# Optimization experiments

Hardware: AMD Instinct MI355X
Metric: run time of the kernel (lower is better)

The kernel has to match this reference:

```python
import jax, jax.numpy as jnp
import numpy as np

B, S, D, H = 2, 2048, 1024, 16
HD = D // H
NEG = -9e15


def setup_inputs() -> dict:
    key = jax.random.key(0)
    ks = jax.random.split(key, 4)
    x = jax.random.normal(ks[0], (B, S, D), dtype=jnp.float32)
    # causal mask, broadcastable over batch and heads
    mask = jnp.tril(jnp.ones((S, S), dtype=jnp.int32))[None, None]
    W_qkv = jax.random.normal(ks[1], (D, 3 * D), dtype=jnp.float32) * (1.0 / np.sqrt(D))
    b_qkv = jnp.zeros((3 * D,), dtype=jnp.float32)
    W_out = jax.random.normal(ks[2], (D, D), dtype=jnp.float32) * (1.0 / np.sqrt(D))
    b_out = jnp.zeros((D,), dtype=jnp.float32)
    return {"x": x, "mask": mask, "W_qkv": W_qkv, "b_qkv": b_qkv,
            "W_out": W_out, "b_out": b_out}


def reference(x, mask, W_qkv, b_qkv, W_out, b_out):
    b, s, _ = x.shape
    qkv = x @ W_qkv + b_qkv                       # [B,S,3D]
    qkv = qkv.reshape(b, s, H, 3 * HD)            # per-head interleaved qkv
    qkv = jnp.transpose(qkv, (0, 2, 1, 3))        # [B,H,S,3*HD]
    q, k, v = jnp.split(qkv, 3, axis=-1)          # each [B,H,S,HD]
    scores = jnp.einsum('bhqd,bhkd->bhqk', q, k) / np.sqrt(HD)
    scores = jnp.where(mask == 0, jnp.float32(NEG), scores)
    attn = jax.nn.softmax(scores, axis=-1)
    out = jnp.einsum('bhqk,bhkd->bhqd', attn, v)  # [B,H,S,HD]
    out = jnp.transpose(out, (0, 2, 1, 3)).reshape(b, s, H * HD)
    return out @ W_out + b_out
```

## Files before the change

kernel.cpp:

```cpp
#include <hip/hip_runtime.h>
#include <math.h>

constexpr int Bb = 2, Ss = 2048, Dd = 1024, Hh = 16, HDd = 64;

typedef __attribute__((ext_vector_type(8))) short bf16x8;
typedef __attribute__((ext_vector_type(4))) float f32x4;
typedef __attribute__((ext_vector_type(8))) unsigned short u16x8;
typedef __attribute__((ext_vector_type(4))) unsigned short u16x4;

__device__ __forceinline__ unsigned short bf16_rn(float f) {
  unsigned int u = __float_as_uint(f);
  u += 0x7fffu + ((u >> 16) & 1u);
  return (unsigned short)(u >> 16);
}
__device__ __forceinline__ float bf16_f(unsigned short h) {
  return __uint_as_float(((unsigned int)h) << 16);
}

__global__ __launch_bounds__(256) void split_f32(
    const float* __restrict__ in, unsigned short* __restrict__ hi,
    unsigned short* __restrict__ lo, int n8) {
  int i = blockIdx.x * 256 + threadIdx.x;
  if (i >= n8) return;
  const float4* p = (const float4*)in + (size_t)i * 2;
  float4 a = p[0], b = p[1];
  float v[8] = {a.x, a.y, a.z, a.w, b.x, b.y, b.z, b.w};
  u16x8 h, l;
  #pragma unroll
  for (int j = 0; j < 8; j++) {
    unsigned short hb = bf16_rn(v[j]);
    h[j] = hb;
    l[j] = bf16_rn(v[j] - bf16_f(hb));
  }
  *(u16x8*)(hi + (size_t)i * 8) = h;
  *(u16x8*)(lo + (size_t)i * 8) = l;
}

__global__ __launch_bounds__(256) void transpose_split_f32(
    const float* __restrict__ W, unsigned short* __restrict__ Thi,
    unsigned short* __restrict__ Tlo, int K, int N) {
  __shared__ float tile[32][33];
  int n0 = blockIdx.x * 32, k0 = blockIdx.y * 32;
  int t = threadIdx.x;
  #pragma unroll
  for (int p = 0; p < 4; p++) {
    int idx = t + p * 256;
    int kk = idx >> 5, nn = idx & 31;
    tile[kk][nn] = W[(size_t)(k0 + kk) * N + n0 + nn];
  }
  __syncthreads();
  #pragma unroll
  for (int p = 0; p < 4; p++) {
    int idx = t + p * 256;
    int nn = idx >> 5, kk = idx & 31;
    float v = tile[kk][nn];
    unsigned short hb = bf16_rn(v);
    size_t o = (size_t)(n0 + nn) * K + k0 + kk;
    Thi[o] = hb;
    Tlo[o] = bf16_rn(v - bf16_f(hb));
  }
}

typedef __attribute__((address_space(3))) unsigned int lds_u32;
typedef const __attribute__((address_space(1))) unsigned int glb_u32;
__device__ __forceinline__ void gload16(const void* g, void* l) {
  __builtin_amdgcn_global_load_lds((glb_u32*)g, (lds_u32*)l, 16, 0, 0);
}

#define GEMM_CORE(KD)                                                          \
  __shared__ unsigned short lds[4 * 4096];                                     \
  const int tid = threadIdx.x;                                                 \
  const int lane = tid & 63, wid = tid >> 6;                                   \
  const int m0 = blockIdx.y * 128, n0 = blockIdx.x * 128;                      \
  const int wrow = wid >> 1, wcol = wid & 1;                                   \
  const int lrow = lane & 15, g = lane >> 4;                                   \
  const int o0 = wid * 128 + lane, o1 = o0 + 64;                               \
  const int r0 = o0 >> 2, G0 = (o0 & 3) ^ ((r0 >> 1) & 3);                     \
  const int r1 = o1 >> 2, G1 = (o1 & 3) ^ ((r1 >> 1) & 3);                     \
  const unsigned short* sA0h = Ahi + (size_t)(m0 + r0) * KD + G0 * 8;          \
  const unsigned short* sA1h = Ahi + (size_t)(m0 + r1) * KD + G1 * 8;          \
  const unsigned short* sA0l = Alo + (size_t)(m0 + r0) * KD + G0 * 8;          \
  const unsigned short* sA1l = Alo + (size_t)(m0 + r1) * KD + G1 * 8;          \
  const unsigned short* sB0h = Bhi + (size_t)(n0 + r0) * KD + G0 * 8;          \
  const unsigned short* sB1h = Bhi + (size_t)(n0 + r1) * KD + G1 * 8;          \
  const unsigned short* sB0l = Blo + (size_t)(n0 + r0) * KD + G0 * 8;          \
  const unsigned short* sB1l = Blo + (size_t)(n0 + r1) * KD + G1 * 8;          \
  unsigned short* dA0h = lds + 0 + wid * 1024;                                 \
  unsigned short* dA1h = dA0h + 512;                                           \
  unsigned short* dA0l = lds + 4096 + wid * 1024;                              \
  unsigned short* dA1l = dA0l + 512;                                           \
  unsigned short* dB0h = lds + 8192 + wid * 1024;                              \
  unsigned short* dB1h = dB0h + 512;                                           \
  unsigned short* dB0l = lds + 12288 + wid * 1024;                             \
  unsigned short* dB1l = dB0l + 512;                                           \
  int offA[4], offB[4];                                                        \
  _Pragma("unroll")                                                            \
  for (int m = 0; m < 4; m++) {                                                \
    int row = wrow * 64 + m * 16 + lrow;                                       \
    offA[m] = row * 32 + ((g ^ ((row >> 1) & 3)) * 8);                         \
  }                                                                            \
  _Pragma("unroll")                                                            \
  for (int n = 0; n < 4; n++) {                                                \
    int row = wcol * 64 + n * 16 + lrow;                                       \
    offB[n] = row * 32 + ((g ^ ((row >> 1) & 3)) * 8);                         \
  }                                                                            \
  f32x4 acc[4][4];                                                             \
  _Pragma("unroll")                                                            \
  for (int m = 0; m < 4; m++)                                                  \
    _Pragma("unroll")                                                          \
    for (int n = 0; n < 4; n++) acc[m][n] = (f32x4){0.f, 0.f, 0.f, 0.f};       \
  for (int k0 = 0; k0 < KD; k0 += 32) {                                        \
    gload16(sA0h + k0, dA0h); gload16(sA1h + k0, dA1h);                        \
    gload16(sA0l + k0, dA0l); gload16(sA1l + k0, dA1l);                        \
    gload16(sB0h + k0, dB0h); gload16(sB1h + k0, dB1h);                        \
    gload16(sB0l + k0, dB0l); gload16(sB1l + k0, dB1l);                        \
    __syncthreads();                                                           \
    bf16x8 ah[4], al[4], bh[4], bl[4];                                         \
    _Pragma("unroll")                                                          \
    for (int m = 0; m < 4; m++) {                                              \
      ah[m] = *(const bf16x8*)(lds + 0 + offA[m]);                             \
      al[m] = *(const bf16x8*)(lds + 4096 + offA[m]);                          \
    }                                                                          \
    _Pragma("unroll")                                                          \
    for (int n = 0; n < 4; n++) {                                              \
      bh[n] = *(const bf16x8*)(lds + 8192 + offB[n]);                          \
      bl[n] = *(const bf16x8*)(lds + 12288 + offB[n]);                         \
    }                                                                          \
    _Pragma("unroll")                                                          \
    for (int m = 0; m < 4; m++)                                                \
      _Pragma("unroll")                                                        \
      for (int n = 0; n < 4; n++) {                                            \
        acc[m][n] = __builtin_amdgcn_mfma_f32_16x16x32_bf16(ah[m], bh[n], acc[m][n], 0, 0, 0); \
        acc[m][n] = __builtin_amdgcn_mfma_f32_16x16x32_bf16(ah[m], bl[n], acc[m][n], 0, 0, 0); \
        acc[m][n] = __builtin_amdgcn_mfma_f32_16x16x32_bf16(al[m], bh[n], acc[m][n], 0, 0, 0); \
      }                                                                        \
    __syncthreads();                                                           \
  }

template<int KD>
__global__ __launch_bounds__(256) void gemm_split_bf16(
    const unsigned short* __restrict__ Ahi, const unsigned short* __restrict__ Alo,
    const unsigned short* __restrict__ Bhi, const unsigned short* __restrict__ Blo,
    const float* __restrict__ bias, float* __restrict__ C, int N)
{
  GEMM_CORE(KD)
  #pragma unroll
  for (int n = 0; n < 4; n++) {
    int gcol = n0 + wcol * 64 + n * 16 + lrow;
    float bv = bias[gcol];
    #pragma unroll
    for (int m = 0; m < 4; m++) {
      f32x4 a = acc[m][n];
      #pragma unroll
      for (int r = 0; r < 4; r++) {
        int grow = m0 + wrow * 64 + m * 16 + g * 4 + r;
        C[(size_t)grow * N + gcol] = a[r] + bv;
      }
    }
  }
}

template<int KD>
__global__ __launch_bounds__(256) void gemm_qkv(
    const unsigned short* __restrict__ Ahi, const unsigned short* __restrict__ Alo,
    const unsigned short* __restrict__ Bhi, const unsigned short* __restrict__ Blo,
    const float* __restrict__ bias,
    unsigned short* __restrict__ Qh, unsigned short* __restrict__ Ql,
    unsigned short* __restrict__ Kh, unsigned short* __restrict__ Kl,
    unsigned short* __restrict__ Vth, unsigned short* __restrict__ Vtl)
{
  GEMM_CORE(KD)
  const int bidx = m0 >> 11;
  const int sbase = (m0 & 2047) + wrow * 64 + g * 4;
  #pragma unroll
  for (int n = 0; n < 4; n++) {
    int gcol = n0 + wcol * 64 + n * 16 + lrow;
    unsigned hh = (unsigned)gcol / 192u;
    int inner = gcol - (int)hh * 192;
    int part = inner >> 6;
    int d = inner & 63;
    float bv = bias[gcol];
    size_t base = (size_t)(bidx * 16 + (int)hh) * 131072;
    #pragma unroll
    for (int m = 0; m < 4; m++) {
      f32x4 a = acc[m][n];
      int s0 = sbase + m * 16;
      if (part == 0) {
        #pragma unroll
        for (int r = 0; r < 4; r++) {
          float v = (a[r] + bv) * 0.18033688011112042f;
          unsigned short hi = bf16_rn(v);
          size_t ix = base + (size_t)(s0 + r) * 64 + d;
          Qh[ix] = hi; Ql[ix] = bf16_rn(v - bf16_f(hi));
        }
      } else if (part == 1) {
        #pragma unroll
        for (int r = 0; r < 4; r++) {
          float v = a[r] + bv;
          unsigned short hi = bf16_rn(v);
          size_t ix = base + (size_t)(s0 + r) * 64 + d;
          Kh[ix] = hi; Kl[ix] = bf16_rn(v - bf16_f(hi));
        }
      } else {
        u16x4 hv, lv;
        #pragma unroll
        for (int r = 0; r < 4; r++) {
          float v = a[r] + bv;
          hv[r] = bf16_rn(v);
          lv[r] = bf16_rn(v - bf16_f(hv[r]));
        }
        size_t ix = base + (size_t)d * 2048 + s0;
        *(u16x4*)(Vth + ix) = hv;
        *(u16x4*)(Vtl + ix) = lv;
      }
    }
  }
}

__global__ __launch_bounds__(256) void flash_attn_mfma(
    const unsigned short* __restrict__ Qh, const unsigned short* __restrict__ Ql,
    const unsigned short* __restrict__ Kh, const unsigned short* __restrict__ Kl,
    const unsigned short* __restrict__ Vth, const unsigned short* __restrict__ Vtl,
    unsigned short* __restrict__ atthi, unsigned short* __restrict__ attlo)
{
  const int qt = (int)gridDim.x - 1 - (int)blockIdx.x;
  const int h = blockIdx.y, b = blockIdx.z;
  const int bh = b * Hh + h;
  const int q0 = qt * 128;
  const int tid = threadIdx.x, lane = tid & 63, wid = tid >> 6;
  const int q0w = q0 + wid * 32;
  const int lrow = lane & 15, lg = lane >> 4;

  __shared__ unsigned short KH[2][4096], KL[2][4096], VH[2][4096], VL[2][4096];
  __shared__ unsigned short Pbuf[4][2048];

  const size_t hb = (size_t)bh * 131072;
  const unsigned short* qhb = Qh + hb;
  const unsigned short* qlb = Ql + hb;
  const unsigned short* khb = Kh + hb;
  const unsigned short* klb = Kl + hb;
  const unsigned short* vhb = Vth + hb;
  const unsigned short* vlb = Vtl + hb;

  bf16x8 qfh[2][2], qfl[2][2];
  #pragma unroll
  for (int mi = 0; mi < 2; mi++)
    #pragma unroll
    for (int ks = 0; ks < 2; ks++) {
      int off = (q0w + mi * 16 + lrow) * 64 + ks * 32 + lg * 8;
      qfh[mi][ks] = *(const bf16x8*)(qhb + off);
      qfl[mi][ks] = *(const bf16x8*)(qlb + off);
    }

  int offK[4][2], offP[2][2];
  #pragma unroll
  for (int ci = 0; ci < 4; ci++)
    #pragma unroll
    for (int ks = 0; ks < 2; ks++) {
      int row = ci * 16 + lrow;
      offK[ci][ks] = row * 64 + (((ks * 4 + lg) ^ (row & 7)) * 8);
    }
  #pragma unroll
  for (int mi = 0; mi < 2; mi++)
    #pragma unroll
    for (int ks = 0; ks < 2; ks++) {
      int row = mi * 16 + lrow;
      offP[mi][ks] = row * 64 + (((ks * 4 + lg) ^ (row & 7)) * 8);
    }

  const int o0 = tid, o1 = tid + 256;
  const int sr0 = o0 >> 3, sg0 = ((o0 & 7) ^ (sr0 & 7)) * 8;
  const int sr1 = o1 >> 3, sg1 = ((o1 & 7) ^ (sr1 & 7)) * 8;

  float m_[2][4], l_[2][4];
  f32x4 oacc[2][4];
  #pragma unroll
  for (int mi = 0; mi < 2; mi++)
    #pragma unroll
    for (int r = 0; r < 4; r++) { m_[mi][r] = -INFINITY; l_[mi][r] = 0.f; }
  #pragma unroll
  for (int mi = 0; mi < 2; mi++)
    #pragma unroll
    for (int di = 0; di < 4; di++) oacc[mi][di] = (f32x4){0.f, 0.f, 0.f, 0.f};

  unsigned short* Pw = Pbuf[wid];
  const int nt = (q0 + 128) >> 6;

  {
    gload16(khb + (size_t)sr0 * 64 + sg0, KH[0] + wid * 512);
    gload16(khb + (size_t)sr1 * 64 + sg1, KH[0] + 2048 + wid * 512);
    gload16(klb + (size_t)sr0 * 64 + sg0, KL[0] + wid * 512);
    gload16(klb + (size_t)sr1 * 64 + sg1, KL[0] + 2048 + wid * 512);
    gload16(vhb + (size_t)sr0 * 2048 + sg0, VH[0] + wid * 512);
    gload16(vhb + (size_t)sr1 * 2048 + sg1, VH[0] + 2048 + wid * 512);
    gload16(vlb + (size_t)sr0 * 2048 + sg0, VL[0] + wid * 512);
    gload16(vlb + (size_t)sr1 * 2048 + sg1, VL[0] + 2048 + wid * 512);
  }
  __syncthreads();

  for (int t = 0; t < nt; ++t) {
    const int kv0 = t * 64;
    if (t + 1 < nt) {
      const int nb = (t + 1) & 1;
      const int nk = kv0 + 64;
      gload16(khb + (size_t)(nk + sr0) * 64 + sg0, KH[nb] + wid * 512);
      gload16(khb + (size_t)(nk + sr1) * 64 + sg1, KH[nb] + 2048 + wid * 512);
      gload16(klb + (size_t)(nk + sr0) * 64 + sg0, KL[nb] + wid * 512);
      gload16(klb + (size_t)(nk + sr1) * 64 + sg1, KL[nb] + 2048 + wid * 512);
      gload16(vhb + (size_t)sr0 * 2048 + nk + sg0, VH[nb] + wid * 512);
      gload16(vhb + (size_t)sr1 * 2048 + nk + sg1, VH[nb] + 2048 + wid * 512);
      gload16(vlb + (size_t)sr0 * 2048 + nk + sg0, VL[nb] + wid * 512);
      gload16(vlb + (size_t)sr1 * 2048 + nk + sg1, VL[nb] + 2048 + wid * 512);
    }

    if (kv0 <= q0w + 31) {
      const int cb = t & 1;
      const unsigned short* KHc = KH[cb];
      const unsigned short* KLc = KL[cb];
      const unsigned short* VHc = VH[cb];
      const unsigned short* VLc = VL[cb];

      f32x4 sf[2][4];
      #pragma unroll
      for (int mi = 0; mi < 2; mi++)
        #pragma unroll
        for (int ci = 0; ci < 4; ci++) sf[mi][ci] = (f32x4){0.f, 0.f, 0.f, 0.f};
      __builtin_amdgcn_s_setprio(1);
      #pragma unroll
      for (int ci = 0; ci < 4; ci++) {
        bf16x8 kh0 = *(const bf16x8*)(KHc + offK[ci][0]);
        bf16x8 kh1 = *(const bf16x8*)(KHc + offK[ci][1]);
        bf16x8 kl0 = *(const bf16x8*)(KLc + offK[ci][0]);
        bf16x8 kl1 = *(const bf16x8*)(KLc + offK[ci][1]);
        #pragma unroll
        for (int mi = 0; mi < 2; mi++) {
          f32x4 s = sf[mi][ci];
          s = __builtin_amdgcn_mfma_f32_16x16x32_bf16(qfh[mi][0], kh0, s, 0, 0, 0);
          s = __builtin_amdgcn_mfma_f32_16x16x32_bf16(qfh[mi][1], kh1, s, 0, 0, 0);
          s = __builtin_amdgcn_mfma_f32_16x16x32_bf16(qfh[mi][0], kl0, s, 0, 0, 0);
          s = __builtin_amdgcn_mfma_f32_16x16x32_bf16(qfh[mi][1], kl1, s, 0, 0, 0);
          s = __builtin_amdgcn_mfma_f32_16x16x32_bf16(qfl[mi][0], kh0, s, 0, 0, 0);
          s = __builtin_amdgcn_mfma_f32_16x16x32_bf16(qfl[mi][1], kh1, s, 0, 0, 0);
          sf[mi][ci] = s;
        }
      }
      __builtin_amdgcn_s_setprio(0);

      if (kv0 + 63 > q0w) {
        #pragma unroll
        for (int mi = 0; mi < 2; mi++)
          #pragma unroll
          for (int ci = 0; ci < 4; ci++)
            #pragma unroll
            for (int r = 0; r < 4; r++) {
              int q = q0w + mi * 16 + lg * 4 + r;
              int kv = kv0 + ci * 16 + lrow;
              if (kv > q) sf[mi][ci][r] = -1e30f;
            }
      }

      #pragma unroll
      for (int mi = 0; mi < 2; mi++)
        #pragma unroll
        for (int r = 0; r < 4; r++) {
          float mx = fmaxf(fmaxf(sf[mi][0][r], sf[mi][1][r]),
                           fmaxf(sf[mi][2][r], sf[mi][3][r]));
          mx = fmaxf(mx, __shfl_xor(mx, 1));
          mx = fmaxf(mx, __shfl_xor(mx, 2));
          mx = fmaxf(mx, __shfl_xor(mx, 4));
          mx = fmaxf(mx, __shfl_xor(mx, 8));
          float mn = fmaxf(m_[mi][r], mx);
          float alpha = __builtin_amdgcn_exp2f(m_[mi][r] - mn);
          m_[mi][r] = mn;
          float rs = 0.f;
          #pragma unroll
          for (int ci = 0; ci < 4; ci++) {
            float p = __builtin_amdgcn_exp2f(sf[mi][ci][r] - mn);
            sf[mi][ci][r] = p;
            rs += p;
          }
          rs += __shfl_xor(rs, 1);
          rs += __shfl_xor(rs, 2);
          rs += __shfl_xor(rs, 4);
          rs += __shfl_xor(rs, 8);
          l_[mi][r] = l_[mi][r] * alpha + rs;
          #pragma unroll
          for (int di = 0; di < 4; di++) oacc[mi][di][r] *= alpha;
        }

      #pragma unroll
      for (int mi = 0; mi < 2; mi++)
        #pragma unroll
        for (int ci = 0; ci < 4; ci++) {
          int colb = ci * 16 + lrow;
          int gcol = colb >> 3, crem = colb & 7;
          #pragma unroll
          for (int r = 0; r < 4; r++) {
            int rr = mi * 16 + lg * 4 + r;
            Pw[rr * 64 + ((gcol ^ (rr & 7)) * 8) + crem] = bf16_rn(sf[mi][ci][r]);
          }
        }

      bf16x8 pa[2][2];
      #pragma unroll
      for (int mi = 0; mi < 2; mi++)
        #pragma unroll
        for (int ks = 0; ks < 2; ks++)
          pa[mi][ks] = *(const bf16x8*)(Pw + offP[mi][ks]);
      __builtin_amdgcn_s_setprio(1);
      #pragma unroll
      for (int di = 0; di < 4; di++) {
        bf16x8 vh0 = *(const bf16x8*)(VHc + offK[di][0]);
        bf16x8 vh1 = *(const bf16x8*)(VHc + offK[di][1]);
        bf16x8 vl0 = *(const bf16x8*)(VLc + offK[di][0]);
        bf16x8 vl1 = *(const bf16x8*)(VLc + offK[di][1]);
        #pragma unroll
        for (int mi = 0; mi < 2; mi++) {
          f32x4 o = oacc[mi][di];
          o = __builtin_amdgcn_mfma_f32_16x16x32_bf16(pa[mi][0], vh0, o, 0, 0, 0);
          o = __builtin_amdgcn_mfma_f32_16x16x32_bf16(pa[mi][1], vh1, o, 0, 0, 0);
          o = __builtin_amdgcn_mfma_f32_16x16x32_bf16(pa[mi][0], vl0, o, 0, 0, 0);
          o = __builtin_amdgcn_mfma_f32_16x16x32_bf16(pa[mi][1], vl1, o, 0, 0, 0);
          oacc[mi][di] = o;
        }
      }
      __builtin_amdgcn_s_setprio(0);
    }
    __syncthreads();
  }

  #pragma unroll
  for (int mi = 0; mi < 2; mi++) {
    float inv[4];
    #pragma unroll
    for (int r = 0; r < 4; r++) inv[r] = 1.f / l_[mi][r];
    #pragma unroll
    for (int di = 0; di < 4; di++) {
      f32x4 o = oacc[mi][di];
      #pragma unroll
      for (int r = 0; r < 4; r++) {
        float v = o[r] * inv[r];
        int srow = q0w + mi * 16 + lg * 4 + r;
        size_t idx = ((size_t)b * Ss + srow) * 1024 + h * 64 + di * 16 + lrow;
        unsigned short hi = bf16_rn(v);
        atthi[idx] = hi;
        attlo[idx] = bf16_rn(v - bf16_f(hi));
      }
    }
  }
}

extern "C" void kernel_launch(void* const* d_in, const int* in_sizes, int n_in,
                              void* d_out, int out_size, void* d_ws, size_t ws_size,
                              hipStream_t stream) {
  const float* x    = (const float*)d_in[0];
  const float* Wqkv = (const float*)d_in[2];
  const float* bqkv = (const float*)d_in[3];
  const float* Wout = (const float*)d_in[4];
  const float* bout = (const float*)d_in[5];
  float* out = (float*)d_out;

  char* ws = (char*)d_ws;
  unsigned short* Qh  = (unsigned short*)(ws);
  unsigned short* Ql  = (unsigned short*)(ws + 8388608);
  unsigned short* Kh  = (unsigned short*)(ws + 16777216);
  unsigned short* Kl  = (unsigned short*)(ws + 25165824);
  unsigned short* Vth = (unsigned short*)(ws + 33554432);
  unsigned short* Vtl = (unsigned short*)(ws + 41943040);
  unsigned short* atthi = (unsigned short*)(ws + 50331648);
  unsigned short* attlo = (unsigned short*)(ws + 58720256);
  unsigned short* xhi = (unsigned short*)(ws + 67108864);
  unsigned short* xlo = (unsigned short*)(ws + 75497472);
  unsigned short* wqh = (unsigned short*)(ws + 83886080);
  unsigned short* wql = (unsigned short*)(ws + 90177536);
  unsigned short* woh = (unsigned short*)(ws + 96468992);
  unsigned short* wol = (unsigned short*)(ws + 98566144);

  const int M = Bb * Ss;

  split_f32<<<(M * Dd / 8) / 256, 256, 0, stream>>>(x, xhi, xlo, M * Dd / 8);
  transpose_split_f32<<<dim3(3 * Dd / 32, Dd / 32), 256, 0, stream>>>(Wqkv, wqh, wql, Dd, 3 * Dd);
  transpose_split_f32<<<dim3(Dd / 32, Dd / 32), 256, 0, stream>>>(Wout, woh, wol, Dd, Dd);

  gemm_qkv<1024><<<dim3(3 * Dd / 128, M / 128), 256, 0, stream>>>(
      xhi, xlo, wqh, wql, bqkv, Qh, Ql, Kh, Kl, Vth, Vtl);

  flash_attn_mfma<<<dim3(Ss / 128, Hh, Bb), 256, 0, stream>>>(
      Qh, Ql, Kh, Kl, Vth, Vtl, atthi, attlo);

  gemm_split_bf16<1024><<<dim3(Dd / 128, M / 128), 256, 0, stream>>>(
      atthi, attlo, woh, wol, bout, out, Dd);
}
```

Before: 385.0 us.

## Pair complementary causal query tiles in one 512-thread attention block

Each flash-attention block now runs 8 waves covering two query tiles, a short early one and the matching long late one, so every block does a balanced amount of causal work and the K/V tiles staged in shared memory are shared by both. Grid size halves and each thread issues one load per buffer instead of two. This is meant to even out per-block work and cut redundant K/V traffic. The cost is larger blocks with more shared memory (Pbuf doubled) and possibly lower occupancy, and waves on the short tile sit idle for the later iterations.

Measured after the change: 355.5 us. -7.7%, faster.

```diff
diff --git a/kernel.cpp b/kernel.cpp
--- a/kernel.cpp
+++ b/kernel.cpp
@@ -217,22 +217,24 @@
   }
 }
 
-__global__ __launch_bounds__(256) void flash_attn_mfma(
+__global__ __launch_bounds__(512) void flash_attn_mfma(
     const unsigned short* __restrict__ Qh, const unsigned short* __restrict__ Ql,
     const unsigned short* __restrict__ Kh, const unsigned short* __restrict__ Kl,
     const unsigned short* __restrict__ Vth, const unsigned short* __restrict__ Vtl,
     unsigned short* __restrict__ atthi, unsigned short* __restrict__ attlo)
 {
-  const int qt = (int)gridDim.x - 1 - (int)blockIdx.x;
+  const int pidx = blockIdx.x;
   const int h = blockIdx.y, b = blockIdx.z;
   const int bh = b * Hh + h;
-  const int q0 = qt * 128;
+  const int NT = Ss / 128;
+  const int qtA = pidx, qtB = NT - 1 - pidx;
   const int tid = threadIdx.x, lane = tid & 63, wid = tid >> 6;
-  const int q0w = q0 + wid * 32;
+  const int q0w = (wid < 4) ? (qtA * 128 + wid * 32)
+                            : (qtB * 128 + (wid - 4) * 32);
   const int lrow = lane & 15, lg = lane >> 4;
 
   __shared__ unsigned short KH[2][4096], KL[2][4096], VH[2][4096], VL[2][4096];
-  __shared__ unsigned short Pbuf[4][2048];
+  __shared__ unsigned short Pbuf[8][2048];
 
   const size_t hb = (size_t)bh * 131072;
   const unsigned short* qhb = Qh + hb;
@@ -268,9 +270,7 @@
       offP[mi][ks] = row * 64 + (((ks * 4 + lg) ^ (row & 7)) * 8);
     }
 
-  const int o0 = tid, o1 = tid + 256;
-  const int sr0 = o0 >> 3, sg0 = ((o0 & 7) ^ (sr0 & 7)) * 8;
-  const int sr1 = o1 >> 3, sg1 = ((o1 & 7) ^ (sr1 & 7)) * 8;
+  const int sr = tid >> 3, sg = ((tid & 7) ^ ((tid >> 3) & 7)) * 8;
 
   float m_[2][4], l_[2][4];
   f32x4 oacc[2][4];
@@ -284,18 +284,12 @@
     for (int di = 0; di < 4; di++) oacc[mi][di] = (f32x4){0.f, 0.f, 0.f, 0.f};
 
   unsigned short* Pw = Pbuf[wid];
-  const int nt = (q0 + 128) >> 6;
-
-  {
-    gload16(khb + (size_t)sr0 * 64 + sg0, KH[0] + wid * 512);
-    gload16(khb + (size_t)sr1 * 64 + sg1, KH[0] + 2048 + wid * 512);
-    gload16(klb + (size_t)sr0 * 64 + sg0, KL[0] + wid * 512);
-    gload16(klb + (size_t)sr1 * 64 + sg1, KL[0] + 2048 + wid * 512);
-    gload16(vhb + (size_t)sr0 * 2048 + sg0, VH[0] + wid * 512);
-    gload16(vhb + (size_t)sr1 * 2048 + sg1, VH[0] + 2048 + wid * 512);
-    gload16(vlb + (size_t)sr0 * 2048 + sg0, VL[0] + wid * 512);
-    gload16(vlb + (size_t)sr1 * 2048 + sg1, VL[0] + 2048 + wid * 512);
-  }
+  const int nt = 2 * (qtB + 1);
+
+  gload16(khb + (size_t)sr * 64 + sg, KH[0] + wid * 512);
+  gload16(klb + (size_t)sr * 64 + sg, KL[0] + wid * 512);
+  gload16(vhb + (size_t)sr * 2048 + sg, VH[0] + wid * 512);
+  gload16(vlb + (size_t)sr * 2048 + sg, VL[0] + wid * 512);
   __syncthreads();
 
   for (int t = 0; t < nt; ++t) {
@@ -303,14 +297,10 @@
     if (t + 1 < nt) {
       const int nb = (t + 1) & 1;
       const int nk = kv0 + 64;
-      gload16(khb + (size_t)(nk + sr0) * 64 + sg0, KH[nb] + wid * 512);
-      gload16(khb + (size_t)(nk + sr1) * 64 + sg1, KH[nb] + 2048 + wid * 512);
-      gload16(klb + (size_t)(nk + sr0) * 64 + sg0, KL[nb] + wid * 512);
-      gload16(klb + (size_t)(nk + sr1) * 64 + sg1, KL[nb] + 2048 + wid * 512);
-      gload16(vhb + (size_t)sr0 * 2048 + nk + sg0, VH[nb] + wid * 512);
-      gload16(vhb + (size_t)sr1 * 2048 + nk + sg1, VH[nb] + 2048 + wid * 512);
-      gload16(vlb + (size_t)sr0 * 2048 + nk + sg0, VL[nb] + wid * 512);
-      gload16(vlb + (size_t)sr1 * 2048 + nk + sg1, VL[nb] + 2048 + wid * 512);
+      gload16(khb + (size_t)(nk + sr) * 64 + sg, KH[nb] + wid * 512);
+      gload16(klb + (size_t)(nk + sr) * 64 + sg, KL[nb] + wid * 512);
+      gload16(vhb + (size_t)sr * 2048 + nk + sg, VH[nb] + wid * 512);
+      gload16(vlb + (size_t)sr * 2048 + nk + sg, VL[nb] + wid * 512);
     }
 
     if (kv0 <= q0w + 31) {
@@ -485,7 +475,7 @@
   gemm_qkv<1024><<<dim3(3 * Dd / 128, M / 128), 256, 0, stream>>>(
       xhi, xlo, wqh, wql, bqkv, Qh, Ql, Kh, Kl, Vth, Vtl);
 
-  flash_attn_mfma<<<dim3(Ss / 128, Hh, Bb), 256, 0, stream>>>(
+  flash_attn_mfma<<<dim3(Ss / 256, Hh, Bb), 512, 0, stream>>>(
       Qh, Ql, Kh, Kl, Vth, Vtl, atthi, attlo);
 
   gemm_split_bf16<1024><<<dim3(Dd / 128, M / 128), 256, 0, stream>>>(
```
